# Performance work log

Measured on AMD Instinct MI355X. Metric: run time of the kernel, lower is better.

The kernel has to match this reference:

```python
import jax, jax.numpy as jnp
import numpy as np

PILLAR_GROUPS = [[0,1,2],[3,4],[5,6],[7,8,9],[10,11],[12,13,14],[15,16],[17,18],[19],[20,21,22],[23,24,25],[26,27,28]]
N_GROUPS = len(PILLAR_GROUPS)      # 12
MAX_G = max(len(g) for g in PILLAR_GROUPS)  # 3
ENC_DIM = 8
EPS = 1e-5

# static padded gather indices + validity mask so all 12 encoders run in one einsum
_idx = np.zeros((N_GROUPS, MAX_G), np.int32)
_msk = np.zeros((N_GROUPS, MAX_G), np.float32)
for _i, _g in enumerate(PILLAR_GROUPS):
    _idx[_i, :len(_g)] = _g
    _msk[_i, :len(_g)] = 1.0
IDX = jnp.asarray(_idx)
MASK = jnp.asarray(_msk)


def bn(h, gamma, beta, mean, var):
    # BatchNorm1d in eval mode (running statistics)
    return gamma * (h - mean) * jax.lax.rsqrt(var + EPS) + beta


def setup_inputs() -> dict:
    key = jax.random.key(0)
    ks = jax.random.split(key, 40)
    B = 524288

    def rn(k, shape, s=0.2):
        return jax.random.normal(k, shape, jnp.float32) * s

    def bn_params(k, d):
        k1, k2, k3, k4 = jax.random.split(k, 4)
        return (1.0 + rn(k1, (d,), 0.05),          # gamma
                rn(k2, (d,), 0.05),                 # beta
                rn(k3, (d,), 0.1),                  # running_mean
                0.5 + jax.random.uniform(k4, (d,), jnp.float32))  # running_var > 0

    g1, bb1, m1, v1 = bn_params(ks[10], 64)
    g2, bb2, m2, v2 = bn_params(ks[11], 32)
    g3, bb3, m3, v3 = bn_params(ks[12], 16)
    eg, ebt, em, ev = bn_params(ks[13], ENC_DIM)
    # per-encoder BN params: [12, 8]
    eg = jnp.tile(eg, (N_GROUPS, 1)) + rn(ks[14], (N_GROUPS, ENC_DIM), 0.02)
    ebt = jnp.tile(ebt, (N_GROUPS, 1)) + rn(ks[15], (N_GROUPS, ENC_DIM), 0.02)
    em = jnp.tile(em, (N_GROUPS, 1)) + rn(ks[16], (N_GROUPS, ENC_DIM), 0.02)
    ev = jnp.tile(ev, (N_GROUPS, 1)) + 0.1 * jax.random.uniform(ks[17], (N_GROUPS, ENC_DIM))

    return {
        "x": jax.random.normal(ks[0], (B, 29), jnp.float32),
        "We": rn(ks[1], (N_GROUPS, MAX_G, ENC_DIM)),  # padded; pad rows hit zeroed x
        "be": rn(ks[2], (N_GROUPS, ENC_DIM)),
        "enc_gamma": eg, "enc_beta": ebt, "enc_mean": em, "enc_var": ev,
        "Wa": rn(ks[3], (ENC_DIM * N_GROUPS, N_GROUPS)),
        "ba": rn(ks[4], (N_GROUPS,)),
        "W1": rn(ks[5], (ENC_DIM * N_GROUPS, 64)), "b1": rn(ks[6], (64,)),
        "g1": g1, "bb1": bb1, "m1": m1, "v1": v1,
        "W2": rn(ks[7], (64, 32)), "b2": rn(ks[8], (32,)),
        "g2": g2, "bb2": bb2, "m2": m2, "v2": v2,
        "W3": rn(ks[9], (32, 16)), "b3": rn(ks[18], (16,)),
        "g3": g3, "bb3": bb3, "m3": m3, "v3": v3,
        "W4": rn(ks[19], (16, 1)), "b4": rn(ks[20], (1,)),
    }


def reference(x, We, be, enc_gamma, enc_beta, enc_mean, enc_var,
              Wa, ba, W1, b1, g1, bb1, m1, v1,
              W2, b2, g2, bb2, m2, v2,
              W3, b3, g3, bb3, m3, v3, W4, b4):
    B = x.shape[0]
    # gather each pillar group (padded to MAX_G, pads zeroed) -> [B, 12, 3]
    xg = x[:, IDX] * MASK
    # all 12 encoders: Linear + ReLU + BN(eval)  -> reps [B, 12, 8]
    reps = jax.nn.relu(jnp.einsum('bgi,gio->bgo', xg, We) + be)
    reps = bn(reps, enc_gamma, enc_beta, enc_mean, enc_var)
    stacked = reps.reshape(B, -1)                      # [B, 96] (cat order matches)
    weights = jax.nn.softmax(stacked @ Wa + ba, axis=1)  # [B, 12]
    attended = (reps * weights[:, :, None]).reshape(B, -1)  # [B, 96]
    h = bn(jax.nn.relu(attended @ W1 + b1), g1, bb1, m1, v1)  # dropout = identity (eval)
    h = bn(jax.nn.relu(h @ W2 + b2), g2, bb2, m2, v2)
    h = bn(jax.nn.relu(h @ W3 + b3), g3, bb3, m3, v3)
    return jax.nn.sigmoid(h @ W4 + b4)[:, 0]           # squeeze(1) -> [B]
```

## Files before the change

### kernel.cpp

```cpp
#include <hip/hip_runtime.h>
#include <math.h>


typedef _Float16 f16x8 __attribute__((ext_vector_type(8)));
typedef float    f32x4 __attribute__((ext_vector_type(4)));

#define EPS 1e-5f

__device__ __forceinline__ float rcp_fast(float v) { return __builtin_amdgcn_rcpf(v); }

__host__ __device__ constexpr unsigned long long packGS() {
    constexpr int gs[12] = {0,3,5,7,10,12,15,17,19,20,23,26};
    unsigned long long v = 0;
    for (int g = 0; g < 12; ++g) v |= (unsigned long long)gs[g] << (5*g);
    return v;
}
__host__ __device__ constexpr unsigned packGL() {
    constexpr int gl[12] = {3,2,2,3,2,3,2,2,1,3,3,3};
    unsigned v = 0;
    for (int g = 0; g < 12; ++g) v |= (unsigned)gl[g] << (2*g);
    return v;
}

__global__ __launch_bounds__(256, 2) void fused_kernel(
    const float* __restrict__ x,
    const float* __restrict__ We,  const float* __restrict__ be,
    const float* __restrict__ eg,  const float* __restrict__ ebt,
    const float* __restrict__ em,  const float* __restrict__ ev,
    const float* __restrict__ Wa,  const float* __restrict__ ba,
    const float* __restrict__ W1,  const float* __restrict__ b1,
    const float* __restrict__ g1,  const float* __restrict__ bb1,
    const float* __restrict__ m1,  const float* __restrict__ v1,
    const float* __restrict__ W2,  const float* __restrict__ b2,
    const float* __restrict__ g2,  const float* __restrict__ bb2,
    const float* __restrict__ m2,  const float* __restrict__ v2,
    const float* __restrict__ W3,  const float* __restrict__ b3,
    const float* __restrict__ g3,  const float* __restrict__ bb3,
    const float* __restrict__ m3,  const float* __restrict__ v3,
    const float* __restrict__ W4,  const float* __restrict__ b4,
    float* __restrict__ out, int B, int ntiles)
{
    __shared__ __align__(16) char smem_raw[32768];
    const int lane = threadIdx.x & 63;
    const int wave = threadIdx.x >> 6;
    const int l15  = lane & 15;
    const int quad = lane >> 4;

    char* sw = smem_raw + wave * 8192;
    _Float16* repT = (_Float16*)(sw);
    float*    wT   = (float*)   (sw + 3328);
    _Float16* h1T  = (_Float16*)(sw + 4416);
    _Float16* h2T  = (_Float16*)(sw + 6720);

    constexpr unsigned long long GS = packGS();
    constexpr unsigned GL = packGL();

    f16x8 Benc[6];
    #pragma unroll
    for (int t = 0; t < 6; ++t) {
        const int n = t*16 + l15;
        const int g = n >> 3, o = n & 7;
        const int gs = (int)((GS >> (5*g)) & 31);
        const int gl = (int)((GL >> (2*g)) & 3);
        #pragma unroll
        for (int j = 0; j < 8; ++j) {
            const int k  = quad*8 + j;
            const int ji = k - gs;
            float v = (ji >= 0 && ji < gl) ? We[(g*3 + ji)*8 + o] : 0.f;
            Benc[t][j] = (_Float16)v;
        }
    }
    f16x8 Bwa[3];
    #pragma unroll
    for (int s = 0; s < 3; ++s) {
        #pragma unroll
        for (int j = 0; j < 8; ++j) {
            const int k = s*32 + quad*8 + j;
            float v = (l15 < 12) ? Wa[k*12 + l15] : 0.f;
            Bwa[s][j] = (_Float16)v;
        }
    }
    f16x8 Bw1[12];
    #pragma unroll
    for (int t = 0; t < 4; ++t)
        #pragma unroll
        for (int s = 0; s < 3; ++s)
            #pragma unroll
            for (int j = 0; j < 8; ++j) {
                const int k = s*32 + quad*8 + j;
                Bw1[t*3 + s][j] = (_Float16)W1[k*64 + t*16 + l15];
            }
    f16x8 Bw2[4];
    #pragma unroll
    for (int t = 0; t < 2; ++t)
        #pragma unroll
        for (int s = 0; s < 2; ++s)
            #pragma unroll
            for (int j = 0; j < 8; ++j) {
                const int k = s*32 + quad*8 + j;
                Bw2[t*2 + s][j] = (_Float16)W2[k*32 + t*16 + l15];
            }
    f16x8 Bw3;
    #pragma unroll
    for (int j = 0; j < 8; ++j)
        Bw3[j] = (_Float16)W3[(quad*8 + j)*16 + l15];

    float encB[6], encS[6], encT[6];
    #pragma unroll
    for (int t = 0; t < 6; ++t) {
        const int c = t*16 + l15;
        float s = eg[c] * rsqrtf(ev[c] + EPS);
        encS[t] = s; encT[t] = ebt[c] - em[c]*s; encB[t] = be[c];
    }
    const float baL = (l15 < 12) ? ba[l15] : -1e4f;
    float b1L[4], s1L[4], t1L[4];
    #pragma unroll
    for (int t = 0; t < 4; ++t) {
        const int c = t*16 + l15;
        float s = g1[c] * rsqrtf(v1[c] + EPS);
        s1L[t] = s; t1L[t] = bb1[c] - m1[c]*s; b1L[t] = b1[c];
    }
    float b2L[2], s2L[2], t2L[2];
    #pragma unroll
    for (int t = 0; t < 2; ++t) {
        const int c = t*16 + l15;
        float s = g2[c] * rsqrtf(v2[c] + EPS);
        s2L[t] = s; t2L[t] = bb2[c] - m2[c]*s; b2L[t] = b2[c];
    }
    const float sv3 = g3[l15] * rsqrtf(v3[l15] + EPS);
    const float b3L = b3[l15], s3L = sv3, t3L = bb3[l15] - m3[l15]*sv3;
    const float w4L = W4[l15];
    const float b4v = b4[0];

    const int tile0 = blockIdx.x * 32;
    int tile1 = tile0 + 32; if (tile1 > ntiles) tile1 = ntiles;

    for (int tile = tile0 + wave; tile < tile1; tile += 4) {
        const int rowbase = tile << 4;

        int xr = rowbase + l15; if (xr > B-1) xr = B-1;
        const float* xp = x + (size_t)xr*29 + quad*8;
        float xv[8];
        if (quad < 3) {
            #pragma unroll
            for (int j = 0; j < 8; ++j) xv[j] = xp[j];
        } else {
            #pragma unroll
            for (int j = 0; j < 5; ++j) xv[j] = xp[j];
            xv[5] = xv[6] = xv[7] = 0.f;
        }
        f16x8 ax;
        #pragma unroll
        for (int j = 0; j < 8; ++j) ax[j] = (_Float16)xv[j];

        #pragma unroll
        for (int t = 0; t < 6; ++t) {
            f32x4 c = { encB[t], encB[t], encB[t], encB[t] };
            c = __builtin_amdgcn_mfma_f32_16x16x32_f16(ax, Benc[t], c, 0, 0, 0);
            #pragma unroll
            for (int r = 0; r < 4; ++r) {
                float v = fmaf(fmaxf(c[r], 0.f), encS[t], encT[t]);
                repT[(quad*4 + r)*104 + t*16 + l15] = (_Float16)v;
            }
        }

        f32x4 c2 = { baL, baL, baL, baL };
        #pragma unroll
        for (int s = 0; s < 3; ++s) {
            f16x8 a = *(const f16x8*)(repT + l15*104 + s*32 + quad*8);
            c2 = __builtin_amdgcn_mfma_f32_16x16x32_f16(a, Bwa[s], c2, 0, 0, 0);
        }
        #pragma unroll
        for (int r = 0; r < 4; ++r) {
            float v = c2[r];
            float mx = v;
            mx = fmaxf(mx, __shfl_xor(mx, 1));
            mx = fmaxf(mx, __shfl_xor(mx, 2));
            mx = fmaxf(mx, __shfl_xor(mx, 4));
            mx = fmaxf(mx, __shfl_xor(mx, 8));
            float e = __expf(v - mx);
            float sm = e;
            sm += __shfl_xor(sm, 1);
            sm += __shfl_xor(sm, 2);
            sm += __shfl_xor(sm, 4);
            sm += __shfl_xor(sm, 8);
            wT[(quad*4 + r)*17 + l15] = e * rcp_fast(sm);
        }

        f32x4 c3[4];
        #pragma unroll
        for (int t = 0; t < 4; ++t) c3[t] = { b1L[t], b1L[t], b1L[t], b1L[t] };
        #pragma unroll
        for (int s = 0; s < 3; ++s) {
            f16x8 a = *(const f16x8*)(repT + l15*104 + s*32 + quad*8);
            _Float16 wh = (_Float16)wT[l15*17 + s*4 + quad];
            f16x8 aw;
            #pragma unroll
            for (int j = 0; j < 8; ++j) aw[j] = a[j] * wh;
            #pragma unroll
            for (int t = 0; t < 4; ++t)
                c3[t] = __builtin_amdgcn_mfma_f32_16x16x32_f16(aw, Bw1[t*3 + s], c3[t], 0, 0, 0);
        }
        #pragma unroll
        for (int t = 0; t < 4; ++t)
            #pragma unroll
            for (int r = 0; r < 4; ++r) {
                float v = fmaf(fmaxf(c3[t][r], 0.f), s1L[t], t1L[t]);
                h1T[(quad*4 + r)*72 + t*16 + l15] = (_Float16)v;
            }

        f32x4 c4[2];
        #pragma unroll
        for (int t = 0; t < 2; ++t) c4[t] = { b2L[t], b2L[t], b2L[t], b2L[t] };
        #pragma unroll
        for (int s = 0; s < 2; ++s) {
            f16x8 a = *(const f16x8*)(h1T + l15*72 + s*32 + quad*8);
            #pragma unroll
            for (int t = 0; t < 2; ++t)
                c4[t] = __builtin_amdgcn_mfma_f32_16x16x32_f16(a, Bw2[t*2 + s], c4[t], 0, 0, 0);
        }
        #pragma unroll
        for (int t = 0; t < 2; ++t)
            #pragma unroll
            for (int r = 0; r < 4; ++r) {
                float v = fmaf(fmaxf(c4[t][r], 0.f), s2L[t], t2L[t]);
                h2T[(quad*4 + r)*40 + t*16 + l15] = (_Float16)v;
            }

        f32x4 c5 = { b3L, b3L, b3L, b3L };
        {
            f16x8 a = *(const f16x8*)(h2T + l15*40 + quad*8);
            c5 = __builtin_amdgcn_mfma_f32_16x16x32_f16(a, Bw3, c5, 0, 0, 0);
        }

        float z[4];
        #pragma unroll
        for (int r = 0; r < 4; ++r) {
            float v = fmaf(fmaxf(c5[r], 0.f), s3L, t3L);
            float p = v * w4L;
            p += __shfl_xor(p, 1);
            p += __shfl_xor(p, 2);
            p += __shfl_xor(p, 4);
            p += __shfl_xor(p, 8);
            z[r] = p;
        }
        float zi = (l15 == 0) ? z[0] : (l15 == 1) ? z[1] : (l15 == 2) ? z[2] : z[3];
        if (l15 < 4) {
            int row = rowbase + quad*4 + l15;
            if (row < B)
                out[row] = rcp_fast(1.f + __expf(-(zi + b4v)));
        }
    }
}

extern "C" void kernel_launch(void* const* d_in, const int* in_sizes, int n_in,
                              void* d_out, int out_size, void* d_ws, size_t ws_size,
                              hipStream_t stream)
{
    const float* x   = (const float*)d_in[0];
    const float* We  = (const float*)d_in[1];
    const float* be  = (const float*)d_in[2];
    const float* eg  = (const float*)d_in[3];
    const float* ebt = (const float*)d_in[4];
    const float* em  = (const float*)d_in[5];
    const float* ev  = (const float*)d_in[6];
    const float* Wa  = (const float*)d_in[7];
    const float* ba  = (const float*)d_in[8];
    const float* W1  = (const float*)d_in[9];
    const float* b1  = (const float*)d_in[10];
    const float* g1  = (const float*)d_in[11];
    const float* bb1 = (const float*)d_in[12];
    const float* m1  = (const float*)d_in[13];
    const float* v1  = (const float*)d_in[14];
    const float* W2  = (const float*)d_in[15];
    const float* b2  = (const float*)d_in[16];
    const float* g2  = (const float*)d_in[17];
    const float* bb2 = (const float*)d_in[18];
    const float* m2  = (const float*)d_in[19];
    const float* v2  = (const float*)d_in[20];
    const float* W3  = (const float*)d_in[21];
    const float* b3  = (const float*)d_in[22];
    const float* g3  = (const float*)d_in[23];
    const float* bb3 = (const float*)d_in[24];
    const float* m3  = (const float*)d_in[25];
    const float* v3  = (const float*)d_in[26];
    const float* W4  = (const float*)d_in[27];
    const float* b4  = (const float*)d_in[28];

    const int B = in_sizes[0] / 29;
    const int ntiles = (B + 15) / 16;
    const int blocks = (ntiles + 31) / 32;

    fused_kernel<<<blocks, 256, 0, stream>>>(
        x, We, be, eg, ebt, em, ev, Wa, ba,
        W1, b1, g1, bb1, m1, v1,
        W2, b2, g2, bb2, m2, v2,
        W3, b3, g3, bb3, m3, v3,
        W4, b4, (float*)d_out, B, ntiles);
}
```

Before: 197.8 us.

## Prefetch next tile's x rows, raise occupancy, halve tiles per block

```diff
diff --git a/kernel.cpp b/kernel.cpp
--- a/kernel.cpp
+++ b/kernel.cpp
@@ -22,7 +22,7 @@
     return v;
 }
 
-__global__ __launch_bounds__(256, 2) void fused_kernel(
+__global__ __launch_bounds__(256, 3) void fused_kernel(
     const float* __restrict__ x,
     const float* __restrict__ We,  const float* __restrict__ be,
     const float* __restrict__ eg,  const float* __restrict__ ebt,
@@ -132,23 +132,36 @@
     const float w4L = W4[l15];
     const float b4v = b4[0];
 
-    const int tile0 = blockIdx.x * 32;
-    int tile1 = tile0 + 32; if (tile1 > ntiles) tile1 = ntiles;
-
-    for (int tile = tile0 + wave; tile < tile1; tile += 4) {
+    const int tile0 = blockIdx.x * 16;
+    int tile1 = tile0 + 16; if (tile1 > ntiles) tile1 = ntiles;
+
+    auto load_x = [&](int t, float* d) {
+        const int rb = t << 4;
+        int xr = rb + l15; if (xr > B-1) xr = B-1;
+        const float* xp = x + (size_t)xr*29 + (quad<<3);
+        if (quad < 3) {
+            #pragma unroll
+            for (int j = 0; j < 8; ++j) d[j] = xp[j];
+        } else {
+            #pragma unroll
+            for (int j = 0; j < 5; ++j) d[j] = xp[j];
+            d[5] = d[6] = d[7] = 0.f;
+        }
+    };
+
+    float xv[8];
+    int tile = tile0 + wave;
+    if (tile < tile1) load_x(tile, xv);
+
+    for (; tile < tile1; tile += 4) {
         const int rowbase = tile << 4;
 
-        int xr = rowbase + l15; if (xr > B-1) xr = B-1;
-        const float* xp = x + (size_t)xr*29 + quad*8;
-        float xv[8];
-        if (quad < 3) {
-            #pragma unroll
-            for (int j = 0; j < 8; ++j) xv[j] = xp[j];
-        } else {
-            #pragma unroll
-            for (int j = 0; j < 5; ++j) xv[j] = xp[j];
-            xv[5] = xv[6] = xv[7] = 0.f;
-        }
+        float xn[8];
+        {
+            int nt = tile + 4;
+            load_x(nt < tile1 ? nt : tile, xn);
+        }
+
         f16x8 ax;
         #pragma unroll
         for (int j = 0; j < 8; ++j) ax[j] = (_Float16)xv[j];
@@ -164,12 +177,15 @@
             }
         }
 
+        f16x8 aS[3];
+        #pragma unroll
+        for (int s = 0; s < 3; ++s)
+            aS[s] = *(const f16x8*)(repT + l15*104 + s*32 + quad*8);
+
         f32x4 c2 = { baL, baL, baL, baL };
         #pragma unroll
-        for (int s = 0; s < 3; ++s) {
-            f16x8 a = *(const f16x8*)(repT + l15*104 + s*32 + quad*8);
-            c2 = __builtin_amdgcn_mfma_f32_16x16x32_f16(a, Bwa[s], c2, 0, 0, 0);
-        }
+        for (int s = 0; s < 3; ++s)
+            c2 = __builtin_amdgcn_mfma_f32_16x16x32_f16(aS[s], Bwa[s], c2, 0, 0, 0);
         #pragma unroll
         for (int r = 0; r < 4; ++r) {
             float v = c2[r];
@@ -192,11 +208,10 @@
         for (int t = 0; t < 4; ++t) c3[t] = { b1L[t], b1L[t], b1L[t], b1L[t] };
         #pragma unroll
         for (int s = 0; s < 3; ++s) {
-            f16x8 a = *(const f16x8*)(repT + l15*104 + s*32 + quad*8);
             _Float16 wh = (_Float16)wT[l15*17 + s*4 + quad];
             f16x8 aw;
             #pragma unroll
-            for (int j = 0; j < 8; ++j) aw[j] = a[j] * wh;
+            for (int j = 0; j < 8; ++j) aw[j] = aS[s][j] * wh;
             #pragma unroll
             for (int t = 0; t < 4; ++t)
                 c3[t] = __builtin_amdgcn_mfma_f32_16x16x32_f16(aw, Bw1[t*3 + s], c3[t], 0, 0, 0);
@@ -250,6 +265,9 @@
             if (row < B)
                 out[row] = rcp_fast(1.f + __expf(-(zi + b4v)));
         }
+
+        #pragma unroll
+        for (int j = 0; j < 8; ++j) xv[j] = xn[j];
     }
 }
 
@@ -289,7 +307,7 @@
 
     const int B = in_sizes[0] / 29;
     const int ntiles = (B + 15) / 16;
-    const int blocks = (ntiles + 31) / 32;
+    const int blocks = (ntiles + 15) / 16;
 
     fused_kernel<<<blocks, 256, 0, stream>>>(
         x, We, be, eg, ebt, em, ev, Wa, ba,
```

Result: slower. 474.2 us (+139.7%).
